# Kernel tuning notes

Measured on AMD Instinct MI355X. Metric: run time of the kernel, lower is better.

Reference implementation:

```python
import jax, jax.numpy as jnp
import numpy as np

D_MODEL = 1024
NUM_HEADS = 16
D_K = D_MODEL // NUM_HEADS


def setup_inputs() -> dict:
    key = jax.random.key(0)
    ks = jax.random.split(key, 11)
    B, S = 4, 2048
    s = 1.0 / np.sqrt(D_MODEL)
    return {
        "Q": jax.random.normal(ks[0], (B, S, D_MODEL), jnp.float32),
        "K": jax.random.normal(ks[1], (B, S, D_MODEL), jnp.float32),
        "V": jax.random.normal(ks[2], (B, S, D_MODEL), jnp.float32),
        "Wq": jax.random.normal(ks[3], (D_MODEL, D_MODEL), jnp.float32) * s,
        "bq": jax.random.normal(ks[4], (D_MODEL,), jnp.float32) * 0.01,
        "Wk": jax.random.normal(ks[5], (D_MODEL, D_MODEL), jnp.float32) * s,
        "bk": jax.random.normal(ks[6], (D_MODEL,), jnp.float32) * 0.01,
        "Wv": jax.random.normal(ks[7], (D_MODEL, D_MODEL), jnp.float32) * s,
        "bv": jax.random.normal(ks[8], (D_MODEL,), jnp.float32) * 0.01,
        "Wo": jax.random.normal(ks[9], (D_MODEL, D_MODEL), jnp.float32) * s,
        "bo": jax.random.normal(ks[10], (D_MODEL,), jnp.float32) * 0.01,
    }


def _split_heads(x):
    B, S, _ = x.shape
    return x.reshape(B, S, NUM_HEADS, D_K).transpose(0, 2, 1, 3)  # [B,H,S,Dk]


def reference(Q, K, V, Wq, bq, Wk, bk, Wv, bv, Wo, bo):
    # Linear layers (torch nn.Linear: x @ W.T + b)
    q = _split_heads(Q @ Wq.T + bq)
    k = _split_heads(K @ Wk.T + bk)
    v = _split_heads(V @ Wv.T + bv)
    scale = 1.0 / jnp.sqrt(jnp.asarray(D_K, jnp.float32))
    scores = jnp.einsum('bhqd,bhkd->bhqk', q, k) * scale  # [B,H,S,S]
    attn = jax.nn.softmax(scores, axis=-1)
    ctx = jnp.einsum('bhqk,bhkd->bhqd', attn, v)  # [B,H,S,Dk]
    B, H, S, Dk = ctx.shape
    ctx = ctx.transpose(0, 2, 1, 3).reshape(B, S, H * Dk)
    return ctx @ Wo.T + bo
```

## Files before the change

kernel.cpp:

```cpp
#include <hip/hip_runtime.h>
#include <hip/hip_bf16.h>

#define B_SZ 4
#define S_SZ 2048
#define D_SZ 1024
#define H_SZ 16
#define DK_SZ 64
#define M_ROWS (B_SZ * S_SZ)

typedef __bf16 bf16x8 __attribute__((ext_vector_type(8)));
typedef __bf16 bf16x4 __attribute__((ext_vector_type(4)));
typedef float  f32x4  __attribute__((ext_vector_type(4)));

typedef __attribute__((address_space(3))) unsigned int lds_u32;
typedef const __attribute__((address_space(1))) unsigned int glob_u32;

__device__ __forceinline__ bf16x8 load8(const float* p) {
    f32x4 a = *(const f32x4*)p;
    f32x4 b = *(const f32x4*)(p + 4);
    bf16x8 r;
    r[0] = (__bf16)a[0]; r[1] = (__bf16)a[1]; r[2] = (__bf16)a[2]; r[3] = (__bf16)a[3];
    r[4] = (__bf16)b[0]; r[5] = (__bf16)b[1]; r[6] = (__bf16)b[2]; r[7] = (__bf16)b[3];
    return r;
}
__device__ __forceinline__ bf16x8 load8(const __bf16* p) {
    return *(const bf16x8*)p;
}

__global__ __launch_bounds__(256)
void conv_bf16(const float* __restrict__ in, __bf16* __restrict__ out, int n8) {
    int i = blockIdx.x * 256 + threadIdx.x;
    const int stride = gridDim.x * 256;
    for (; i < n8; i += stride)
        *(bf16x8*)&out[(size_t)i * 8] = load8(in + (size_t)i * 8);
}

template <typename TC>
__global__ __launch_bounds__(256, 2)
void gemm_nt_bias_g(const __bf16* __restrict__ A, const __bf16* __restrict__ W,
                    const float* __restrict__ bias, TC* __restrict__ C,
                    int M, int N, int K) {
    __shared__ __align__(16) __bf16 sA[2][128 * 64];
    __shared__ __align__(16) __bf16 sB[2][128 * 64];
    const int tid = threadIdx.x;
    const int w = tid >> 6, lane = tid & 63;

    int mt, nt;
    if (gridDim.x == 64 && gridDim.y == 8) {
        const int lin = blockIdx.x + blockIdx.y * 64;
        const int xcd = lin & 7, idx = lin >> 3;
        mt = xcd * 8 + (idx >> 3);
        nt = idx & 7;
    } else { mt = blockIdx.x; nt = blockIdx.y; }
    const int m0 = mt * 128, n0 = nt * 128;

    const int wr = w >> 1, wc = w & 1;
    const int lr = lane & 15, lq = lane >> 4;

    const int st_roff = lane >> 3;
    const int st_cg   = (lane & 7) ^ st_roff;

    f32x4 acc[4][4] = {};

    auto STAGE = [&](int kt, int bsel) {
#pragma unroll
        for (int i = 0; i < 4; ++i) {
            const int seg = i * 4 + w;
            const int row = seg * 8 + st_roff;
            __builtin_amdgcn_global_load_lds(
                (glob_u32*)(A + (size_t)(m0 + row) * K + kt + st_cg * 8),
                (lds_u32*)(&sA[bsel][seg * 512]), 16, 0, 0);
            __builtin_amdgcn_global_load_lds(
                (glob_u32*)(W + (size_t)(n0 + row) * K + kt + st_cg * 8),
                (lds_u32*)(&sB[bsel][seg * 512]), 16, 0, 0);
        }
    };
    auto COMPUTE = [&](int bsel) {
#pragma unroll
        for (int s = 0; s < 2; ++s) {
            bf16x8 av[4], bv[4];
#pragma unroll
            for (int i = 0; i < 4; ++i)
                av[i] = *(const bf16x8*)&sA[bsel][(wr * 64 + i * 16 + lr) * 64
                                                  + (((s * 4 + lq) ^ (lr & 7)) << 3)];
#pragma unroll
            for (int j = 0; j < 4; ++j)
                bv[j] = *(const bf16x8*)&sB[bsel][(wc * 64 + j * 16 + lr) * 64
                                                  + (((s * 4 + lq) ^ (lr & 7)) << 3)];
#pragma unroll
            for (int i = 0; i < 4; ++i)
#pragma unroll
                for (int j = 0; j < 4; ++j)
                    acc[i][j] = __builtin_amdgcn_mfma_f32_16x16x32_bf16(
                        av[i], bv[j], acc[i][j], 0, 0, 0);
        }
    };

    STAGE(0, 0);
    STAGE(64, 1);
    int buf = 0;
    for (int kt = 0; kt + 64 < K; kt += 64) {
        asm volatile("s_waitcnt vmcnt(8)" ::: "memory");
        __builtin_amdgcn_s_barrier();
        COMPUTE(buf);
        __builtin_amdgcn_s_barrier();
        if (kt + 128 < K) STAGE(kt + 128, buf);
        buf ^= 1;
    }
    asm volatile("s_waitcnt vmcnt(0)" ::: "memory");
    __builtin_amdgcn_s_barrier();
    COMPUTE(buf);

#pragma unroll
    for (int j = 0; j < 4; ++j) {
        const int col = n0 + wc * 64 + j * 16 + lr;
        const float bias_f = bias[col];
#pragma unroll
        for (int i = 0; i < 4; ++i) {
            const int rbase = m0 + wr * 64 + i * 16 + lq * 4;
#pragma unroll
            for (int r = 0; r < 4; ++r)
                C[(size_t)(rbase + r) * N + col] = (TC)(acc[i][j][r] + bias_f);
        }
    }
}

#define SAST 72
template <typename TA, typename TW, typename TC>
__global__ __launch_bounds__(256, 2)
void gemm_nt_bias(const TA* __restrict__ A, const TW* __restrict__ W,
                  const float* __restrict__ bias, TC* __restrict__ C,
                  int M, int N, int K) {
    __shared__ __align__(16) __bf16 sA[128 * SAST];
    __shared__ __align__(16) __bf16 sB[128 * SAST];
    const int tid = threadIdx.x;
    const int w = tid >> 6, lane = tid & 63;
    const int m0 = blockIdx.x * 128, n0 = blockIdx.y * 128;
    const int wr = w >> 1, wc = w & 1;
    const int lr = lane & 15, lq = lane >> 4;

    f32x4 acc[4][4] = {};

    for (int kt = 0; kt < K; kt += 64) {
        for (int it = 0; it < 4; ++it) {
            const int c = it * 256 + tid;
            const int row = c >> 3, col8 = c & 7;
            *(bf16x8*)&sA[row * SAST + col8 * 8] =
                load8(A + (size_t)(m0 + row) * K + kt + col8 * 8);
            *(bf16x8*)&sB[row * SAST + col8 * 8] =
                load8(W + (size_t)(n0 + row) * K + kt + col8 * 8);
        }
        __syncthreads();
        for (int s = 0; s < 2; ++s) {
            bf16x8 av[4], bv[4];
            for (int i = 0; i < 4; ++i)
                av[i] = *(const bf16x8*)&sA[(wr * 64 + i * 16 + lr) * SAST + s * 32 + lq * 8];
            for (int j = 0; j < 4; ++j)
                bv[j] = *(const bf16x8*)&sB[(wc * 64 + j * 16 + lr) * SAST + s * 32 + lq * 8];
            for (int i = 0; i < 4; ++i)
                for (int j = 0; j < 4; ++j)
                    acc[i][j] = __builtin_amdgcn_mfma_f32_16x16x32_bf16(
                        av[i], bv[j], acc[i][j], 0, 0, 0);
        }
        __syncthreads();
    }
    for (int j = 0; j < 4; ++j) {
        const int col = n0 + wc * 64 + j * 16 + lr;
        const float bias_f = bias[col];
        for (int i = 0; i < 4; ++i) {
            const int rbase = m0 + wr * 64 + i * 16 + lq * 4;
            for (int r = 0; r < 4; ++r)
                C[(size_t)(rbase + r) * N + col] = (TC)(acc[i][j][r] + bias_f);
        }
    }
}

#define KVB 64
__global__ __launch_bounds__(256, 4)
void attn_kernel(const __bf16* qm, const __bf16* __restrict__ km,
                 const __bf16* __restrict__ vm, __bf16* ctx) {
    __shared__ __align__(16) __bf16 sK[2][KVB * 64];
    __shared__ __align__(16) __bf16 sVt[2][64 * KVB];
    __shared__ __align__(16) __bf16 sP[4][16 * 64];

    const int tid = threadIdx.x, w = tid >> 6, lane = tid & 63;
    const int lr = lane & 15, lq = lane >> 4;

    int qblk, bh;
    if (gridDim.x == 16 && gridDim.y == 64) {
        const int lin = blockIdx.x + blockIdx.y * 16;
        const int xcd = lin & 7, idx = lin >> 3;
        bh = xcd * 8 + (idx >> 4);
        qblk = idx & 15;
    } else { qblk = blockIdx.x; bh = blockIdx.y; }
    const int b = bh >> 4, h = bh & 15;
    const int q0 = qblk * 128;
    const size_t rowbase = (size_t)b * S_SZ;
    const int hoff = h * DK_SZ;

    bf16x8 qf[2][2];
#pragma unroll
    for (int qs = 0; qs < 2; ++qs) {
        const __bf16* qp = qm + (rowbase + q0 + w * 32 + qs * 16 + lr) * D_SZ + hoff;
        qf[qs][0] = *(const bf16x8*)(qp + lq * 8);
        qf[qs][1] = *(const bf16x8*)(qp + 32 + lq * 8);
    }

    float mrow[2] = {-1e30f, -1e30f};
    float lrow[2] = {0.f, 0.f};
    f32x4 o[2][4] = {};

    const int gl_koff = (lane >> 3);
    const int gl_c8 = lane & 7;
    const int v_key7 = tid >> 3, v_d8 = tid & 7;
    const int cb0 = (((v_key7 >> 3) ^ v_d8) << 3) + (v_key7 & 7);
    const int cb1 = ((((32 + v_key7) >> 3) ^ v_d8) << 3) + (v_key7 & 7);

    const int sp_row = lr * 64;
    const int sp_xor = lr & 7;

    const __bf16* kbase = km + rowbase * D_SZ + hoff;
    const __bf16* vbase = vm + rowbase * D_SZ + hoff;

    auto stageK = [&](int k0t, int bsel) {
#pragma unroll
        for (int i = 0; i < 2; ++i) {
            const int key = w * 16 + i * 8 + gl_koff;
            const __bf16* gp = kbase + (size_t)(k0t + key) * D_SZ
                               + ((gl_c8 ^ gl_koff) << 3);
            __builtin_amdgcn_global_load_lds(
                (glob_u32*)gp, (lds_u32*)(&sK[bsel][(w * 2 + i) * 512]), 16, 0, 0);
        }
    };

    stageK(0, 0);
    {
        bf16x8 a0 = *(const bf16x8*)(vbase + (size_t)(v_key7) * D_SZ + (v_d8 << 3));
        bf16x8 a1 = *(const bf16x8*)(vbase + (size_t)(32 + v_key7) * D_SZ + (v_d8 << 3));
#pragma unroll
        for (int e = 0; e < 8; ++e) {
            sVt[0][(v_d8 * 8 + e) * 64 + cb0] = a0[e];
            sVt[0][(v_d8 * 8 + e) * 64 + cb1] = a1[e];
        }
    }
    __syncthreads();

    int buf = 0;
    for (int k0 = 0; k0 < S_SZ; k0 += KVB) {
        const bool more = (k0 + KVB) < S_SZ;
        bf16x8 nv0, nv1;
        if (more) {
            stageK(k0 + KVB, buf ^ 1);
            nv0 = *(const bf16x8*)(vbase + (size_t)(k0 + KVB + v_key7) * D_SZ + (v_d8 << 3));
            nv1 = *(const bf16x8*)(vbase + (size_t)(k0 + KVB + 32 + v_key7) * D_SZ + (v_d8 << 3));
        }

        bf16x8 pf[2][2];
#pragma unroll
        for (int qs = 0; qs < 2; ++qs) {
            f32x4 sc[4] = {};
#pragma unroll
            for (int s = 0; s < 2; ++s) {
                bf16x8 kf[4];
#pragma unroll
                for (int nt = 0; nt < 4; ++nt)
                    kf[nt] = *(const bf16x8*)&sK[buf][(nt * 16 + lr) * 64
                                                      + (((s * 4 + lq) ^ (lr & 7)) << 3)];
#pragma unroll
                for (int nt = 0; nt < 4; ++nt)
                    sc[nt] = __builtin_amdgcn_mfma_f32_16x16x32_bf16(
                        kf[nt], qf[qs][s], sc[nt], 0, 0, 0);
            }

            float sv[4][4];
            float mt = -1e30f;
#pragma unroll
            for (int nt = 0; nt < 4; ++nt)
#pragma unroll
                for (int r = 0; r < 4; ++r) {
                    sv[nt][r] = sc[nt][r] * 0.125f;
                    mt = fmaxf(mt, sv[nt][r]);
                }
            mt = fmaxf(mt, __shfl_xor(mt, 16));
            mt = fmaxf(mt, __shfl_xor(mt, 32));
            if (!__all(mt - mrow[qs] <= 8.f)) {
                const float mn = fmaxf(mrow[qs], mt);
                const float al = __expf(mrow[qs] - mn);
                mrow[qs] = mn;
                lrow[qs] *= al;
                float a4[4];
#pragma unroll
                for (int r = 0; r < 4; ++r)
                    a4[r] = __shfl(al, ((lane >> 4) << 2) + r, 64);
#pragma unroll
                for (int nt = 0; nt < 4; ++nt)
#pragma unroll
                    for (int r = 0; r < 4; ++r)
                        o[qs][nt][r] *= a4[r];
            }
            float ls = 0.f;
#pragma unroll
            for (int nt = 0; nt < 4; ++nt) {
                bf16x4 pk;
#pragma unroll
                for (int r = 0; r < 4; ++r) {
                    const float pv = __expf(sv[nt][r] - mrow[qs]);
                    ls += pv;
                    pk[r] = (__bf16)pv;
                }
                *(bf16x4*)&sP[w][sp_row
                                 + (((nt * 2 + (lq >> 1)) ^ sp_xor) << 3)
                                 + ((lq & 1) << 2)] = pk;
            }
            ls += __shfl_xor(ls, 16);
            ls += __shfl_xor(ls, 32);
            lrow[qs] += ls;

#pragma unroll
            for (int s = 0; s < 2; ++s)
                pf[qs][s] = *(const bf16x8*)&sP[w][sp_row
                                                   + (((s * 4 + lq) ^ sp_xor) << 3)];
        }

#pragma unroll
        for (int s = 0; s < 2; ++s)
#pragma unroll
            for (int nt = 0; nt < 4; ++nt) {
                bf16x8 vf = *(const bf16x8*)&sVt[buf][
                    (nt * 16 + lr) * 64
                    + (((s * 4 + lq) ^ (nt * 2 + (lr >> 3))) << 3)];
                o[0][nt] = __builtin_amdgcn_mfma_f32_16x16x32_bf16(
                    pf[0][s], vf, o[0][nt], 0, 0, 0);
                o[1][nt] = __builtin_amdgcn_mfma_f32_16x16x32_bf16(
                    pf[1][s], vf, o[1][nt], 0, 0, 0);
            }

        if (more) {
#pragma unroll
            for (int e = 0; e < 8; ++e) {
                sVt[buf ^ 1][(v_d8 * 8 + e) * 64 + cb0] = nv0[e];
                sVt[buf ^ 1][(v_d8 * 8 + e) * 64 + cb1] = nv1[e];
            }
            __syncthreads();
        }
        buf ^= 1;
    }

#pragma unroll
    for (int qs = 0; qs < 2; ++qs) {
        const float linv = 1.f / lrow[qs];
        float l4[4];
#pragma unroll
        for (int r = 0; r < 4; ++r)
            l4[r] = __shfl(linv, ((lane >> 4) << 2) + r, 64);
#pragma unroll
        for (int nt = 0; nt < 4; ++nt) {
            const int col = hoff + nt * 16 + lr;
#pragma unroll
            for (int r = 0; r < 4; ++r) {
                const size_t row = rowbase + q0 + w * 32 + qs * 16 + lq * 4 + r;
                ctx[row * D_SZ + col] = (__bf16)(o[qs][nt][r] * l4[r]);
            }
        }
    }
}

extern "C" void kernel_launch(void* const* d_in, const int* in_sizes, int n_in,
                              void* d_out, int out_size, void* d_ws, size_t ws_size,
                              hipStream_t stream) {
    const float* Q  = (const float*)d_in[0];
    const float* K  = (const float*)d_in[1];
    const float* V  = (const float*)d_in[2];
    const float* Wq = (const float*)d_in[3];
    const float* bq = (const float*)d_in[4];
    const float* Wk = (const float*)d_in[5];
    const float* bk = (const float*)d_in[6];
    const float* Wv = (const float*)d_in[7];
    const float* bv = (const float*)d_in[8];
    const float* Wo = (const float*)d_in[9];
    const float* bo = (const float*)d_in[10];
    float* out = (float*)d_out;

    const size_t plane = (size_t)M_ROWS * D_SZ;
    const size_t wsz   = (size_t)D_SZ * D_SZ;
    const dim3 gg(M_ROWS / 128, D_SZ / 128), bb(256);
    const dim3 ag(S_SZ / 128, B_SZ * H_SZ);

    const size_t need_fast = (3 * plane + 4 * wsz) * sizeof(__bf16);
    if (ws_size >= need_fast) {
        __bf16* s0  = (__bf16*)d_ws;
        __bf16* qw  = s0 + plane;
        __bf16* kw  = s0 + 2 * plane;
        __bf16* wgt = s0 + 3 * plane;
        __bf16* vw  = (__bf16*)d_out;
        const int p8 = (int)(plane / 8), w8 = (int)(wsz / 8);

        conv_bf16<<<512, bb, 0, stream>>>(Wq, wgt, w8);
        conv_bf16<<<512, bb, 0, stream>>>(Wk, wgt + wsz, w8);
        conv_bf16<<<512, bb, 0, stream>>>(Wv, wgt + 2 * wsz, w8);
        conv_bf16<<<512, bb, 0, stream>>>(Wo, wgt + 3 * wsz, w8);

        conv_bf16<<<2048, bb, 0, stream>>>(Q, s0, p8);
        gemm_nt_bias_g<__bf16><<<gg, bb, 0, stream>>>(
            s0, wgt, bq, qw, M_ROWS, D_SZ, D_SZ);
        conv_bf16<<<2048, bb, 0, stream>>>(K, s0, p8);
        gemm_nt_bias_g<__bf16><<<gg, bb, 0, stream>>>(
            s0, wgt + wsz, bk, kw, M_ROWS, D_SZ, D_SZ);
        conv_bf16<<<2048, bb, 0, stream>>>(V, s0, p8);
        gemm_nt_bias_g<__bf16><<<gg, bb, 0, stream>>>(
            s0, wgt + 2 * wsz, bv, vw, M_ROWS, D_SZ, D_SZ);

        attn_kernel<<<ag, bb, 0, stream>>>(qw, kw, vw, qw);

        gemm_nt_bias_g<float><<<gg, bb, 0, stream>>>(
            qw, wgt + 3 * wsz, bo, out, M_ROWS, D_SZ, D_SZ);
        return;
    }

    if (ws_size < 2 * plane * sizeof(__bf16)) return;
    __bf16* qw = (__bf16*)d_ws;
    __bf16* kw = qw + plane;
    __bf16* vw = (__bf16*)d_out;
    __bf16* cw = qw;

    gemm_nt_bias<float, float, __bf16><<<gg, bb, 0, stream>>>(Q, Wq, bq, qw, M_ROWS, D_SZ, D_SZ);
    gemm_nt_bias<float, float, __bf16><<<gg, bb, 0, stream>>>(K, Wk, bk, kw, M_ROWS, D_SZ, D_SZ);
    gemm_nt_bias<float, float, __bf16><<<gg, bb, 0, stream>>>(V, Wv, bv, vw, M_ROWS, D_SZ, D_SZ);

    attn_kernel<<<ag, bb, 0, stream>>>(qw, kw, vw, cw);

    gemm_nt_bias<__bf16, float, float><<<gg, bb, 0, stream>>>(cw, Wo, bo, out,
                                                              M_ROWS, D_SZ, D_SZ);
}
```

Before: 381.6 us.

## Fuse fp32-to-bf16 activation conversion into projection GEMM staging; batch weight conversion

Removes the separate conversion kernels for Q, K and V by letting the projection GEMM read fp32 activations directly, convert them in registers and write them to LDS. The four weight conversions are merged into one launch. This drops a full write and re-read of each bf16 activation plane and several launches. In exchange, the fp32 path loses the async global-to-LDS loads and the vmcnt-based pipelining, using synchronous loads plus __syncthreads, which may expose latency in the GEMM loop.

```diff
diff --git a/kernel.cpp b/kernel.cpp
--- a/kernel.cpp
+++ b/kernel.cpp
@@ -28,16 +28,20 @@
 }
 
 __global__ __launch_bounds__(256)
-void conv_bf16(const float* __restrict__ in, __bf16* __restrict__ out, int n8) {
-    int i = blockIdx.x * 256 + threadIdx.x;
-    const int stride = gridDim.x * 256;
-    for (; i < n8; i += stride)
-        *(bf16x8*)&out[(size_t)i * 8] = load8(in + (size_t)i * 8);
-}
-
-template <typename TC>
+void conv4_bf16(const float* __restrict__ w0, const float* __restrict__ w1,
+                const float* __restrict__ w2, const float* __restrict__ w3,
+                __bf16* __restrict__ out, int wsz_n8) {
+    const int p = blockIdx.x >> 7;
+    const float* src = (p == 0) ? w0 : (p == 1) ? w1 : (p == 2) ? w2 : w3;
+    __bf16* dst = out + (size_t)p * (size_t)wsz_n8 * 8;
+    const int stride = 128 * 256;
+    for (int i = (blockIdx.x & 127) * 256 + threadIdx.x; i < wsz_n8; i += stride)
+        *(bf16x8*)&dst[(size_t)i * 8] = load8(src + (size_t)i * 8);
+}
+
+template <typename TA, typename TC>
 __global__ __launch_bounds__(256, 2)
-void gemm_nt_bias_g(const __bf16* __restrict__ A, const __bf16* __restrict__ W,
+void gemm_nt_bias_g(const TA* __restrict__ A, const __bf16* __restrict__ W,
                     const float* __restrict__ bias, TC* __restrict__ C,
                     int M, int N, int K) {
     __shared__ __align__(16) __bf16 sA[2][128 * 64];
@@ -62,17 +66,34 @@
 
     f32x4 acc[4][4] = {};
 
-    auto STAGE = [&](int kt, int bsel) {
+    auto STAGE_W = [&](int kt, int bsel) {
 #pragma unroll
         for (int i = 0; i < 4; ++i) {
             const int seg = i * 4 + w;
             const int row = seg * 8 + st_roff;
             __builtin_amdgcn_global_load_lds(
-                (glob_u32*)(A + (size_t)(m0 + row) * K + kt + st_cg * 8),
-                (lds_u32*)(&sA[bsel][seg * 512]), 16, 0, 0);
-            __builtin_amdgcn_global_load_lds(
                 (glob_u32*)(W + (size_t)(n0 + row) * K + kt + st_cg * 8),
                 (lds_u32*)(&sB[bsel][seg * 512]), 16, 0, 0);
+        }
+    };
+    auto STAGE_A = [&](int kt, int bsel) {
+        if constexpr (sizeof(TA) == 2) {
+#pragma unroll
+            for (int i = 0; i < 4; ++i) {
+                const int seg = i * 4 + w;
+                const int row = seg * 8 + st_roff;
+                __builtin_amdgcn_global_load_lds(
+                    (glob_u32*)(A + (size_t)(m0 + row) * K + kt + st_cg * 8),
+                    (lds_u32*)(&sA[bsel][seg * 512]), 16, 0, 0);
+            }
+        } else {
+#pragma unroll
+            for (int i = 0; i < 4; ++i) {
+                const int seg = i * 4 + w;
+                const int row = seg * 8 + st_roff;
+                const TA* ap = A + (size_t)(m0 + row) * K + kt + st_cg * 8;
+                *(bf16x8*)&sA[bsel][seg * 512 + lane * 8] = load8(ap);
+            }
         }
     };
     auto COMPUTE = [&](int bsel) {
@@ -96,20 +117,33 @@
         }
     };
 
-    STAGE(0, 0);
-    STAGE(64, 1);
-    int buf = 0;
-    for (int kt = 0; kt + 64 < K; kt += 64) {
-        asm volatile("s_waitcnt vmcnt(8)" ::: "memory");
+    if constexpr (sizeof(TA) == 2) {
+        STAGE_A(0, 0);  STAGE_W(0, 0);
+        STAGE_A(64, 1); STAGE_W(64, 1);
+        int buf = 0;
+        for (int kt = 0; kt + 64 < K; kt += 64) {
+            asm volatile("s_waitcnt vmcnt(8)" ::: "memory");
+            __builtin_amdgcn_s_barrier();
+            COMPUTE(buf);
+            __builtin_amdgcn_s_barrier();
+            if (kt + 128 < K) { STAGE_A(kt + 128, buf); STAGE_W(kt + 128, buf); }
+            buf ^= 1;
+        }
+        asm volatile("s_waitcnt vmcnt(0)" ::: "memory");
         __builtin_amdgcn_s_barrier();
         COMPUTE(buf);
-        __builtin_amdgcn_s_barrier();
-        if (kt + 128 < K) STAGE(kt + 128, buf);
-        buf ^= 1;
-    }
-    asm volatile("s_waitcnt vmcnt(0)" ::: "memory");
-    __builtin_amdgcn_s_barrier();
-    COMPUTE(buf);
+    } else {
+        STAGE_A(0, 0); STAGE_W(0, 0);
+        __syncthreads();
+        int buf = 0;
+        for (int kt = 64; kt < K; kt += 64) {
+            STAGE_A(kt, buf ^ 1); STAGE_W(kt, buf ^ 1);
+            COMPUTE(buf);
+            __syncthreads();
+            buf ^= 1;
+        }
+        COMPUTE(buf);
+    }
 
 #pragma unroll
     for (int j = 0; j < 4; ++j) {
@@ -386,33 +420,26 @@
     const dim3 gg(M_ROWS / 128, D_SZ / 128), bb(256);
     const dim3 ag(S_SZ / 128, B_SZ * H_SZ);
 
-    const size_t need_fast = (3 * plane + 4 * wsz) * sizeof(__bf16);
+    const size_t need_fast = (2 * plane + 4 * wsz) * sizeof(__bf16);
     if (ws_size >= need_fast) {
-        __bf16* s0  = (__bf16*)d_ws;
-        __bf16* qw  = s0 + plane;
-        __bf16* kw  = s0 + 2 * plane;
-        __bf16* wgt = s0 + 3 * plane;
+        __bf16* qw  = (__bf16*)d_ws;
+        __bf16* kw  = qw + plane;
+        __bf16* wgt = qw + 2 * plane;
         __bf16* vw  = (__bf16*)d_out;
-        const int p8 = (int)(plane / 8), w8 = (int)(wsz / 8);
-
-        conv_bf16<<<512, bb, 0, stream>>>(Wq, wgt, w8);
-        conv_bf16<<<512, bb, 0, stream>>>(Wk, wgt + wsz, w8);
-        conv_bf16<<<512, bb, 0, stream>>>(Wv, wgt + 2 * wsz, w8);
-        conv_bf16<<<512, bb, 0, stream>>>(Wo, wgt + 3 * wsz, w8);
-
-        conv_bf16<<<2048, bb, 0, stream>>>(Q, s0, p8);
-        gemm_nt_bias_g<__bf16><<<gg, bb, 0, stream>>>(
-            s0, wgt, bq, qw, M_ROWS, D_SZ, D_SZ);
-        conv_bf16<<<2048, bb, 0, stream>>>(K, s0, p8);
-        gemm_nt_bias_g<__bf16><<<gg, bb, 0, stream>>>(
-            s0, wgt + wsz, bk, kw, M_ROWS, D_SZ, D_SZ);
-        conv_bf16<<<2048, bb, 0, stream>>>(V, s0, p8);
-        gemm_nt_bias_g<__bf16><<<gg, bb, 0, stream>>>(
-            s0, wgt + 2 * wsz, bv, vw, M_ROWS, D_SZ, D_SZ);
+        const int w8 = (int)(wsz / 8);
+
+        conv4_bf16<<<512, bb, 0, stream>>>(Wq, Wk, Wv, Wo, wgt, w8);
+
+        gemm_nt_bias_g<float, __bf16><<<gg, bb, 0, stream>>>(
+            Q, wgt, bq, qw, M_ROWS, D_SZ, D_SZ);
+        gemm_nt_bias_g<float, __bf16><<<gg, bb, 0, stream>>>(
+            K, wgt + wsz, bk, kw, M_ROWS, D_SZ, D_SZ);
+        gemm_nt_bias_g<float, __bf16><<<gg, bb, 0, stream>>>(
+            V, wgt + 2 * wsz, bv, vw, M_ROWS, D_SZ, D_SZ);
 
         attn_kernel<<<ag, bb, 0, stream>>>(qw, kw, vw, qw);
 
-        gemm_nt_bias_g<float><<<gg, bb, 0, stream>>>(
+        gemm_nt_bias_g<__bf16, float><<<gg, bb, 0, stream>>>(
             qw, wgt + 3 * wsz, bo, out, M_ROWS, D_SZ, D_SZ);
         return;
     }
```

Result: slower. 401.9 us (+5.3%).
